# Kernel optimization log

Hardware: AMD Instinct MI355X
Metric: run time of the kernel (lower is better)

Reference implementation:

```python
import jax, jax.numpy as jnp
import numpy as np

H = 768
IMG_DIM = 2048
B = 256
S = 512
EPS = 1e-5


def _ln(x, g, b):
    mu = jnp.mean(x, axis=-1, keepdims=True)
    var = jnp.var(x, axis=-1, keepdims=True)
    return (x - mu) * jax.lax.rsqrt(var + EPS) * g + b


def setup_inputs() -> dict:
    key = jax.random.key(0)
    ks = jax.random.split(key, 16)
    std = 0.02
    d = {
        "text_features": jax.random.normal(ks[0], (B, S, H), jnp.float32),
        "image_features": jax.random.normal(ks[1], (B, IMG_DIM), jnp.float32),
        # projections (stored as [in, out]); attention/proj weights init N(0, 0.02), zero bias
        "Wp": jax.random.normal(ks[2], (IMG_DIM, H), jnp.float32) * std,
        "bp": jnp.zeros((H,), jnp.float32),
        "Wtq": jax.random.normal(ks[3], (H, H), jnp.float32) * std,
        "btq": jnp.zeros((H,), jnp.float32),
        "Wik": jax.random.normal(ks[4], (H, H), jnp.float32) * std,
        "bik": jnp.zeros((H,), jnp.float32),
        "Wiv": jax.random.normal(ks[5], (H, H), jnp.float32) * std,
        "biv": jnp.zeros((H,), jnp.float32),
        "Wiq": jax.random.normal(ks[6], (H, H), jnp.float32) * std,
        "biq": jnp.zeros((H,), jnp.float32),
        "Wtk": jax.random.normal(ks[7], (H, H), jnp.float32) * std,
        "btk": jnp.zeros((H,), jnp.float32),
        "Wtv": jax.random.normal(ks[8], (H, H), jnp.float32) * std,
        "btv": jnp.zeros((H,), jnp.float32),
        # layernorms
        "tn_g": jnp.ones((H,), jnp.float32),
        "tn_b": jnp.zeros((H,), jnp.float32),
        "in_g": jnp.ones((H,), jnp.float32),
        "in_b": jnp.zeros((H,), jnp.float32),
        # fusion MLP: Linear(2H,H) + LN + GELU
        "Wf": jax.random.normal(ks[9], (2 * H, H), jnp.float32) * (1.0 / np.sqrt(2 * H)),
        "bf": jnp.zeros((H,), jnp.float32),
        "fn_g": jnp.ones((H,), jnp.float32),
        "fn_b": jnp.zeros((H,), jnp.float32),
        # gate: Linear(2H,2) + softmax
        "Wg": jax.random.normal(ks[10], (2 * H, 2), jnp.float32) * (1.0 / np.sqrt(2 * H)),
        "bg": jnp.zeros((2,), jnp.float32),
    }
    return d


def reference(text_features, image_features, Wp, bp, Wtq, btq, Wik, bik, Wiv, biv,
              Wiq, biq, Wtk, btk, Wtv, btv, tn_g, tn_b, in_g, in_b,
              Wf, bf, fn_g, fn_b, Wg, bg):
    scale = 1.0 / jnp.sqrt(jnp.float32(H))
    cls_token = text_features[:, 0]                       # [B, H]
    img_projected = image_features @ Wp + bp              # [B, H]

    # image query attends over text tokens
    img_q = img_projected @ Wiq + biq                     # [B, H]
    text_k = jnp.einsum('bsd,de->bse', text_features, Wtk) + btk  # [B, S, H]
    text_v = jnp.einsum('bsd,de->bse', text_features, Wtv) + btv  # [B, S, H]
    scores = jnp.einsum('bd,bsd->bs', img_q, text_k) * scale      # [B, S]
    attn = jax.nn.softmax(scores, axis=-1)
    img_context = jnp.einsum('bs,bsd->bd', attn, text_v)          # [B, H]
    img_context = _ln(img_context + img_projected, in_g, in_b)

    # text CLS query attends over the single image token (softmax over 1 -> weight 1)
    text_q = cls_token @ Wtq + btq                        # [B, H]
    img_k = img_projected @ Wik + bik                     # [B, H]
    img_v = img_projected @ Wiv + biv                     # [B, H]
    t_scores = jnp.sum(text_q * img_k, axis=-1, keepdims=True) * scale  # [B, 1]
    t_attn = jax.nn.softmax(t_scores, axis=-1)            # == 1
    text_context = t_attn * img_v                         # [B, H]
    text_context = _ln(text_context + cls_token, tn_g, tn_b)

    combined = jnp.concatenate([text_context, img_context], axis=1)  # [B, 2H]
    gate = jax.nn.softmax(combined @ Wg + bg, axis=-1)               # [B, 2]
    weighted = jnp.concatenate([text_context * gate[:, 0:1],
                                img_context * gate[:, 1:2]], axis=1)  # [B, 2H]
    out = jax.nn.gelu(_ln(weighted @ Wf + bf, fn_g, fn_b), approximate=False)
    return out
```

## Files before the change

kernel.cpp:

```cpp
#include <hip/hip_runtime.h>
#include <hip/hip_bf16.h>

#define BD   256
#define SD   512
#define HD   768
#define IMGD 2048
#define TWOH 1536
constexpr float EPSV  = 1e-5f;
constexpr float SCALE = 0.036084391824351615f;
constexpr int   SPLIT = 4;
constexpr int   SBLK  = SD / SPLIT;

typedef __attribute__((ext_vector_type(8))) short short8;
typedef __attribute__((ext_vector_type(4))) float f32x4;

__device__ __forceinline__ short f2bs(float x) {
    __hip_bfloat16 h = __float2bfloat16(x);
    return __builtin_bit_cast(short, h);
}
__device__ __forceinline__ float4 f4sum(float4 a, float4 b) {
    return make_float4(a.x + b.x, a.y + b.y, a.z + b.z, a.w + b.w);
}
__device__ __forceinline__ float4 f4fma(float s, float4 v, float4 acc) {
    return make_float4(fmaf(s, v.x, acc.x), fmaf(s, v.y, acc.y),
                       fmaf(s, v.z, acc.z), fmaf(s, v.w, acc.w));
}

struct GemmSmem {
    __hip_bfloat16 As[2][64][40];
    __hip_bfloat16 Bs[2][64][40];
};

template<bool TRANSB, class AF, class BF>
__device__ __forceinline__ void gemm_core(GemmSmem& smem, AF aload, BF bload,
        const float* __restrict__ bias, float* __restrict__ C,
        int N, int m0, int n0, int NT) {
    const int tid  = threadIdx.x;
    const int w    = tid >> 6, lane = tid & 63;
    const int wr   = w >> 1,  wc   = w & 1;
    const int rsel = lane & 15, ks = (lane >> 4) * 8;
    const int arow = tid >> 2, akc = (tid & 3) * 8;
    const int bkk  = tid >> 3, bnc = (tid & 7) * 8;

    float4 a0v[2], a1v[2], b0v[2], b1v[2];

    auto issue = [&](int slot, int t) {
        aload(t, a0v[slot], a1v[slot]);
        bload(t, b0v[slot], b1v[slot]);
    };
    auto commit = [&](int buf, int slot) {
        short8 pk;
        pk[0]=f2bs(a0v[slot].x); pk[1]=f2bs(a0v[slot].y);
        pk[2]=f2bs(a0v[slot].z); pk[3]=f2bs(a0v[slot].w);
        pk[4]=f2bs(a1v[slot].x); pk[5]=f2bs(a1v[slot].y);
        pk[6]=f2bs(a1v[slot].z); pk[7]=f2bs(a1v[slot].w);
        *(short8*)&smem.As[buf][arow][akc] = pk;
        if (TRANSB) {
            short8 qk;
            qk[0]=f2bs(b0v[slot].x); qk[1]=f2bs(b0v[slot].y);
            qk[2]=f2bs(b0v[slot].z); qk[3]=f2bs(b0v[slot].w);
            qk[4]=f2bs(b1v[slot].x); qk[5]=f2bs(b1v[slot].y);
            qk[6]=f2bs(b1v[slot].z); qk[7]=f2bs(b1v[slot].w);
            *(short8*)&smem.Bs[buf][arow][akc] = qk;
        } else {
            smem.Bs[buf][bnc + 0][bkk] = __float2bfloat16(b0v[slot].x);
            smem.Bs[buf][bnc + 1][bkk] = __float2bfloat16(b0v[slot].y);
            smem.Bs[buf][bnc + 2][bkk] = __float2bfloat16(b0v[slot].z);
            smem.Bs[buf][bnc + 3][bkk] = __float2bfloat16(b0v[slot].w);
            smem.Bs[buf][bnc + 4][bkk] = __float2bfloat16(b1v[slot].x);
            smem.Bs[buf][bnc + 5][bkk] = __float2bfloat16(b1v[slot].y);
            smem.Bs[buf][bnc + 6][bkk] = __float2bfloat16(b1v[slot].z);
            smem.Bs[buf][bnc + 7][bkk] = __float2bfloat16(b1v[slot].w);
        }
    };

    f32x4 zero = {0.f, 0.f, 0.f, 0.f};
    f32x4 acc[2][2] = {{zero, zero}, {zero, zero}};

    issue(0, 0);
    commit(0, 0);
    if (NT > 1) issue(1, 1);
    __syncthreads();

    for (int t = 0; t < NT; ++t) {
        const int cur = t & 1;
        short8 A0 = *(const short8*)&smem.As[cur][wr * 32 + rsel][ks];
        short8 A1 = *(const short8*)&smem.As[cur][wr * 32 + 16 + rsel][ks];
        short8 B0 = *(const short8*)&smem.Bs[cur][wc * 32 + rsel][ks];
        short8 B1 = *(const short8*)&smem.Bs[cur][wc * 32 + 16 + rsel][ks];
        if (t + 1 < NT) commit(cur ^ 1, (t + 1) & 1);
        if (t + 2 < NT) issue(cur, t + 2);
        acc[0][0] = __builtin_amdgcn_mfma_f32_16x16x32_bf16(A0, B0, acc[0][0], 0, 0, 0);
        acc[0][1] = __builtin_amdgcn_mfma_f32_16x16x32_bf16(A0, B1, acc[0][1], 0, 0, 0);
        acc[1][0] = __builtin_amdgcn_mfma_f32_16x16x32_bf16(A1, B0, acc[1][0], 0, 0, 0);
        acc[1][1] = __builtin_amdgcn_mfma_f32_16x16x32_bf16(A1, B1, acc[1][1], 0, 0, 0);
        __syncthreads();
    }

    const int colb = lane & 15, rowb = (lane >> 4) * 4;
    #pragma unroll
    for (int fm = 0; fm < 2; ++fm)
        #pragma unroll
        for (int fn = 0; fn < 2; ++fn)
            #pragma unroll
            for (int r = 0; r < 4; ++r) {
                int row = m0 + wr * 32 + fm * 16 + rowb + r;
                int col = n0 + wc * 32 + fn * 16 + colb;
                float v = acc[fm][fn][r];
                if (bias) v += bias[col];
                C[(size_t)row * N + col] = v;
            }
}

__global__ __launch_bounds__(256) void stage1(const float* __restrict__ imgf,
                                              const float* __restrict__ Wp,
                                              const float* __restrict__ bp,
                                              const float* __restrict__ Wiq,
                                              const float* __restrict__ Wtk,
                                              const float* __restrict__ biq,
                                              float* __restrict__ Pp,
                                              float* __restrict__ Wqkp,
                                              float* __restrict__ v1) {
    __shared__ GemmSmem smem;
    const int blk = blockIdx.x, tid = threadIdx.x;
    const int arow = tid >> 2, akc = (tid & 3) * 8;
    const int bkk  = tid >> 3, bnc = (tid & 7) * 8;
    if (blk < 192) {
        const int part = blk / 48, tile = blk % 48;
        const int m0 = (tile / 12) * 64, n0 = (tile % 12) * 64, kbeg = part * 512;
        const float* ap = &imgf[(size_t)(m0 + arow) * IMGD + kbeg + akc];
        const float* bq = &Wp[(size_t)(kbeg + bkk) * HD + n0 + bnc];
        auto al = [&](int t, float4& v0, float4& v1_) {
            const float* p = ap + t * 32;
            v0 = *(const float4*)p; v1_ = *(const float4*)(p + 4);
        };
        auto bl = [&](int t, float4& v0, float4& v1_) {
            const float* p = bq + (size_t)t * 32 * HD;
            v0 = *(const float4*)p; v1_ = *(const float4*)(p + 4);
        };
        gemm_core<false>(smem, al, bl, part == 0 ? bp : nullptr,
                         Pp + (size_t)part * BD * HD, HD, m0, n0, 16);
    } else if (blk < 768) {
        const int b2 = blk - 192, part = b2 / 144, tile = b2 % 144;
        const int m0 = (tile / 12) * 64, n0 = (tile % 12) * 64, kbeg = part * 192;
        const float* ap = &Wiq[(size_t)(m0 + arow) * HD + kbeg + akc];
        const float* bq = &Wtk[(size_t)(n0 + arow) * HD + kbeg + akc];
        auto al = [&](int t, float4& v0, float4& v1_) {
            const float* p = ap + t * 32;
            v0 = *(const float4*)p; v1_ = *(const float4*)(p + 4);
        };
        auto bl = [&](int t, float4& v0, float4& v1_) {
            const float* p = bq + t * 32;
            v0 = *(const float4*)p; v1_ = *(const float4*)(p + 4);
        };
        gemm_core<true>(smem, al, bl, nullptr,
                        Wqkp + (size_t)part * HD * HD, HD, m0, n0, 6);
    } else {
        const int b2 = blk - 768;
        const int w = tid >> 6, lane = tid & 63;
        float bq[12];
        #pragma unroll
        for (int c = 0; c < 12; ++c) bq[c] = biq[c * 64 + lane];
        const int d0 = b2 * 64 + w * 16;
        for (int i = 0; i < 16; ++i) {
            const float* row = &Wtk[(size_t)(d0 + i) * HD];
            float p = 0.f;
            #pragma unroll
            for (int c = 0; c < 12; ++c) p = fmaf(row[c * 64 + lane], bq[c], p);
            #pragma unroll
            for (int off = 32; off > 0; off >>= 1) p += __shfl_xor(p, off);
            if (lane == 0) v1[d0 + i] = p;
        }
    }
}

__global__ __launch_bounds__(256) void stage2(const float* __restrict__ Pp,
                                              const float* __restrict__ Wqkp,
                                              const float* __restrict__ v1,
                                              const float* __restrict__ Wiv,
                                              const float* __restrict__ biv,
                                              float* __restrict__ qtp,
                                              float* __restrict__ ivp) {
    __shared__ GemmSmem smem;
    const int blk = blockIdx.x, tid = threadIdx.x;
    const int arow = tid >> 2, akc = (tid & 3) * 8;
    const int bkk  = tid >> 3, bnc = (tid & 7) * 8;
    const bool isqt = blk < 192;
    const int b2 = isqt ? blk : blk - 192;
    const int part = b2 / 48, tile = b2 % 48;
    const int m0 = (tile / 12) * 64, n0 = (tile % 12) * 64, kbeg = part * 192;

    const float* ap = &Pp[(size_t)(m0 + arow) * HD + kbeg + akc];
    auto al = [&](int t, float4& v0, float4& v1_) {
        const float* p = ap + t * 32;
        float4 x0 = *(const float4*)p, x1 = *(const float4*)(p + 4);
        #pragma unroll
        for (int q = 1; q < 4; ++q) {
            const float* r = p + (size_t)q * BD * HD;
            x0 = f4sum(x0, *(const float4*)r);
            x1 = f4sum(x1, *(const float4*)(r + 4));
        }
        v0 = x0; v1_ = x1;
    };
    if (isqt) {
        const float* bq = &Wqkp[(size_t)(kbeg + bkk) * HD + n0 + bnc];
        auto bl = [&](int t, float4& v0, float4& v1_) {
            const float* p = bq + (size_t)t * 32 * HD;
            float4 x0 = *(const float4*)p, x1 = *(const float4*)(p + 4);
            #pragma unroll
            for (int q = 1; q < 4; ++q) {
                const float* r = p + (size_t)q * HD * HD;
                x0 = f4sum(x0, *(const float4*)r);
                x1 = f4sum(x1, *(const float4*)(r + 4));
            }
            v0 = x0; v1_ = x1;
        };
        gemm_core<false>(smem, al, bl, part == 0 ? v1 : nullptr,
                         qtp + (size_t)part * BD * HD, HD, m0, n0, 6);
    } else {
        const float* bq = &Wiv[(size_t)(kbeg + bkk) * HD + n0 + bnc];
        auto bl = [&](int t, float4& v0, float4& v1_) {
            const float* p = bq + (size_t)t * 32 * HD;
            v0 = *(const float4*)p; v1_ = *(const float4*)(p + 4);
        };
        gemm_core<false>(smem, al, bl, part == 0 ? biv : nullptr,
                         ivp + (size_t)part * BD * HD, HD, m0, n0, 6);
    }
}

__global__ __launch_bounds__(256) void stream_attn(const float* __restrict__ tf,
                                                   const float* __restrict__ qtp,
                                                   float* __restrict__ pacc,
                                                   float* __restrict__ ml) {
    const int tid = threadIdx.x, w = tid >> 6, lane = tid & 63;
    const int item = blockIdx.x;
    const int b = item >> 2, sl = item & 3;
    __shared__ float sacc[4][HD];
    __shared__ float sm_[4], sl_[4];

    float q[12];
    {
        const float* qp = &qtp[b * HD];
        #pragma unroll
        for (int c = 0; c < 3; ++c) {
            float4 v = *(const float4*)&qp[c * 256 + 4 * lane];
            #pragma unroll
            for (int p = 1; p < 4; ++p)
                v = f4sum(v, *(const float4*)&qp[(size_t)p * BD * HD + c * 256 + 4 * lane]);
            q[c*4+0] = v.x; q[c*4+1] = v.y; q[c*4+2] = v.z; q[c*4+3] = v.w;
        }
    }
    float a[12];
    #pragma unroll
    for (int j = 0; j < 12; ++j) a[j] = 0.f;
    float m = -INFINITY, l = 0.f;

    const int r0 = sl * SBLK + w * (SBLK / 4);
    const float* base = &tf[((size_t)b * SD + r0) * HD];

    float tA[12], tB[12];
    auto loadrow = [&](int i, float* t) {
        const float* row = base + (size_t)i * HD;
        #pragma unroll
        for (int c = 0; c < 3; ++c) {
            float4 v = *(const float4*)&row[c * 256 + 4 * lane];
            t[c*4+0] = v.x; t[c*4+1] = v.y; t[c*4+2] = v.z; t[c*4+3] = v.w;
        }
    };
    auto process = [&](const float* t) {
        float p = 0.f;
        #pragma unroll
        for (int j = 0; j < 12; ++j) p = fmaf(t[j], q[j], p);
        #pragma unroll
        for (int off = 32; off > 0; off >>= 1) p += __shfl_xor(p, off);
        float score = p * SCALE;
        float mn = fmaxf(m, score);
        float eo = __expf(m - mn);
        float en = __expf(score - mn);
        l = fmaf(l, eo, en);
        #pragma unroll
        for (int j = 0; j < 12; ++j) a[j] = fmaf(a[j], eo, en * t[j]);
        m = mn;
    };

    loadrow(0, tA);
    for (int i = 0; i < 32; i += 2) {
        loadrow(i + 1, tB);
        process(tA);
        if (i + 2 < 32) loadrow(i + 2, tA);
        process(tB);
    }

    #pragma unroll
    for (int c = 0; c < 3; ++c)
        #pragma unroll
        for (int j = 0; j < 4; ++j)
            sacc[w][c * 256 + 4 * lane + j] = a[c * 4 + j];
    if (lane == 0) { sm_[w] = m; sl_[w] = l; }
    __syncthreads();
    float gm = fmaxf(fmaxf(sm_[0], sm_[1]), fmaxf(sm_[2], sm_[3]));
    float f0 = __expf(sm_[0] - gm), f1 = __expf(sm_[1] - gm);
    float f2 = __expf(sm_[2] - gm), f3 = __expf(sm_[3] - gm);
    float gl = f0 * sl_[0] + f1 * sl_[1] + f2 * sl_[2] + f3 * sl_[3];
    float* outp = &pacc[(size_t)item * HD];
    #pragma unroll
    for (int jj = 0; jj < 3; ++jj) {
        int c = jj * 256 + tid;
        outp[c] = f0 * sacc[0][c] + f1 * sacc[1][c] + f2 * sacc[2][c] + f3 * sacc[3][c];
    }
    if (tid == 0) { ml[item * 2] = gm; ml[item * 2 + 1] = gl; }
}

__global__ __launch_bounds__(256) void gemm_ctxv(const float* __restrict__ pacc,
                                                 const float* __restrict__ ml,
                                                 const float* __restrict__ Wtv,
                                                 const float* __restrict__ btv,
                                                 float* __restrict__ icpp) {
    __shared__ GemmSmem smem;
    __shared__ float wgt[64][SPLIT];
    const int tid = threadIdx.x;
    const int arow = tid >> 2, akc = (tid & 3) * 8;
    const int bkk  = tid >> 3, bnc = (tid & 7) * 8;
    const int part = blockIdx.x / 48, tile = blockIdx.x % 48;
    const int m0 = (tile / 12) * 64, n0 = (tile % 12) * 64, kbeg = part * 192;

    if (tid < 64) {
        const int gr = m0 + tid;
        float mv[SPLIT], lv[SPLIT];
        #pragma unroll
        for (int s = 0; s < SPLIT; ++s) {
            mv[s] = ml[(gr * SPLIT + s) * 2];
            lv[s] = ml[(gr * SPLIT + s) * 2 + 1];
        }
        float mx = fmaxf(fmaxf(mv[0], mv[1]), fmaxf(mv[2], mv[3]));
        float f[SPLIT], gl = 0.f;
        #pragma unroll
        for (int s = 0; s < SPLIT; ++s) { f[s] = __expf(mv[s] - mx); gl += f[s] * lv[s]; }
        float inv = 1.f / gl;
        #pragma unroll
        for (int s = 0; s < SPLIT; ++s) wgt[tid][s] = f[s] * inv;
    }
    __syncthreads();

    const float* ap = &pacc[(size_t)(m0 + arow) * SPLIT * HD + kbeg + akc];
    auto al = [&](int t, float4& v0, float4& v1_) {
        const float* p = ap + t * 32;
        float4 x0 = {0.f, 0.f, 0.f, 0.f}, x1 = {0.f, 0.f, 0.f, 0.f};
        #pragma unroll
        for (int s = 0; s < SPLIT; ++s) {
            float wv = wgt[arow][s];
            const float* r = p + (size_t)s * HD;
            x0 = f4fma(wv, *(const float4*)r, x0);
            x1 = f4fma(wv, *(const float4*)(r + 4), x1);
        }
        v0 = x0; v1_ = x1;
    };
    const float* bq = &Wtv[(size_t)(kbeg + bkk) * HD + n0 + bnc];
    auto bl = [&](int t, float4& v0, float4& v1_) {
        const float* p = bq + (size_t)t * 32 * HD;
        v0 = *(const float4*)p; v1_ = *(const float4*)(p + 4);
    };
    gemm_core<false>(smem, al, bl, part == 0 ? btv : nullptr,
                     icpp + (size_t)part * BD * HD, HD, m0, n0, 6);
}

__global__ __launch_bounds__(256) void gemm_wf(const float* __restrict__ wtd,
                                               const float* __restrict__ Wf,
                                               const float* __restrict__ bf,
                                               float* __restrict__ ybp) {
    __shared__ GemmSmem smem;
    const int tid = threadIdx.x;
    const int arow = tid >> 2, akc = (tid & 3) * 8;
    const int bkk  = tid >> 3, bnc = (tid & 7) * 8;
    const int part = blockIdx.x / 48, tile = blockIdx.x % 48;
    const int m0 = (tile / 12) * 64, n0 = (tile % 12) * 64, kbeg = part * 192;
    const float* ap = &wtd[(size_t)(m0 + arow) * TWOH + kbeg + akc];
    const float* bq = &Wf[(size_t)(kbeg + bkk) * HD + n0 + bnc];
    auto al = [&](int t, float4& v0, float4& v1_) {
        const float* p = ap + t * 32;
        v0 = *(const float4*)p; v1_ = *(const float4*)(p + 4);
    };
    auto bl = [&](int t, float4& v0, float4& v1_) {
        const float* p = bq + (size_t)t * 32 * HD;
        v0 = *(const float4*)p; v1_ = *(const float4*)(p + 4);
    };
    gemm_core<false>(smem, al, bl, part == 0 ? bf : nullptr,
                     ybp + (size_t)part * BD * HD, HD, m0, n0, 6);
}

__device__ __forceinline__ float block_sum256(float v, float* red, int w, int lane) {
    #pragma unroll
    for (int off = 32; off > 0; off >>= 1) v += __shfl_xor(v, off);
    __syncthreads();
    if (lane == 0) red[w] = v;
    __syncthreads();
    return red[0] + red[1] + red[2] + red[3];
}

__global__ __launch_bounds__(256) void fuse_small(const float* __restrict__ icpp,
                                                  const float* __restrict__ Pp,
                                                  const float* __restrict__ ivp,
                                                  const float* __restrict__ tf,
                                                  const float* __restrict__ in_g,
                                                  const float* __restrict__ in_b,
                                                  const float* __restrict__ tn_g,
                                                  const float* __restrict__ tn_b,
                                                  const float* __restrict__ Wg,
                                                  const float* __restrict__ bg,
                                                  float* __restrict__ wtd) {
    const int b = blockIdx.x, tid = threadIdx.x;
    const int w = tid >> 6, lane = tid & 63;
    __shared__ float red[4];
    float icv[3], tcv[3];
    #pragma unroll
    for (int j = 0; j < 3; ++j) {
        int c = j * 256 + tid;
        float pv = 0.f, ic = 0.f, iv = 0.f;
        #pragma unroll
        for (int q = 0; q < 4; ++q) {
            pv += Pp[(size_t)q * BD * HD + b * HD + c];
            ic += icpp[(size_t)q * BD * HD + b * HD + c];
            iv += ivp[(size_t)q * BD * HD + b * HD + c];
        }
        icv[j] = ic + pv;
        tcv[j] = iv + tf[(size_t)b * SD * HD + c];
    }
    float s_i  = block_sum256(icv[0] + icv[1] + icv[2], red, w, lane);
    float ss_i = block_sum256(icv[0]*icv[0] + icv[1]*icv[1] + icv[2]*icv[2], red, w, lane);
    float s_t  = block_sum256(tcv[0] + tcv[1] + tcv[2], red, w, lane);
    float ss_t = block_sum256(tcv[0]*tcv[0] + tcv[1]*tcv[1] + tcv[2]*tcv[2], red, w, lane);
    const float invh = 1.f / HD;
    float mu_i = s_i * invh, var_i = ss_i * invh - mu_i * mu_i;
    float mu_t = s_t * invh, var_t = ss_t * invh - mu_t * mu_t;
    float rs_i = rsqrtf(var_i + EPSV), rs_t = rsqrtf(var_t + EPSV);
    float icn[3], tcn[3];
    #pragma unroll
    for (int j = 0; j < 3; ++j) {
        int c = j * 256 + tid;
        icn[j] = (icv[j] - mu_i) * rs_i * in_g[c] + in_b[c];
        tcn[j] = (tcv[j] - mu_t) * rs_t * tn_g[c] + tn_b[c];
    }
    float z0p = 0.f, z1p = 0.f;
    #pragma unroll
    for (int j = 0; j < 3; ++j) {
        int c = j * 256 + tid;
        z0p += tcn[j] * Wg[c * 2 + 0] + icn[j] * Wg[(HD + c) * 2 + 0];
        z1p += tcn[j] * Wg[c * 2 + 1] + icn[j] * Wg[(HD + c) * 2 + 1];
    }
    float z0 = block_sum256(z0p, red, w, lane) + bg[0];
    float z1 = block_sum256(z1p, red, w, lane) + bg[1];
    float mx = fmaxf(z0, z1);
    float e0 = __expf(z0 - mx), e1 = __expf(z1 - mx);
    float inv = 1.f / (e0 + e1);
    float g0 = e0 * inv, g1 = e1 * inv;
    #pragma unroll
    for (int j = 0; j < 3; ++j) {
        int c = j * 256 + tid;
        wtd[(size_t)b * TWOH + c]      = tcn[j] * g0;
        wtd[(size_t)b * TWOH + HD + c] = icn[j] * g1;
    }
}

__global__ __launch_bounds__(256) void final_ln_gelu(const float* __restrict__ ybp,
                                                     const float* __restrict__ fn_g,
                                                     const float* __restrict__ fn_b,
                                                     float* __restrict__ out) {
    const int b = blockIdx.x, tid = threadIdx.x;
    const int w = tid >> 6, lane = tid & 63;
    __shared__ float red[4];
    float v[3];
    #pragma unroll
    for (int j = 0; j < 3; ++j) {
        int c = j * 256 + tid;
        float x = 0.f;
        #pragma unroll
        for (int q = 0; q < 8; ++q) x += ybp[(size_t)q * BD * HD + b * HD + c];
        v[j] = x;
    }
    float s  = block_sum256(v[0] + v[1] + v[2], red, w, lane);
    float ss = block_sum256(v[0]*v[0] + v[1]*v[1] + v[2]*v[2], red, w, lane);
    const float invh = 1.f / HD;
    float mu = s * invh, var = ss * invh - mu * mu;
    float rs = rsqrtf(var + EPSV);
    #pragma unroll
    for (int j = 0; j < 3; ++j) {
        int c = j * 256 + tid;
        float x = (v[j] - mu) * rs * fn_g[c] + fn_b[c];
        float g = 0.5f * x * (1.f + erff(x * 0.7071067811865476f));
        out[b * HD + c] = g;
    }
}

extern "C" void kernel_launch(void* const* d_in, const int* in_sizes, int n_in,
                              void* d_out, int out_size, void* d_ws, size_t ws_size,
                              hipStream_t stream) {
    const float* tf   = (const float*)d_in[0];
    const float* imgf = (const float*)d_in[1];
    const float* Wp   = (const float*)d_in[2];
    const float* bp   = (const float*)d_in[3];
    const float* Wiv  = (const float*)d_in[8];
    const float* biv  = (const float*)d_in[9];
    const float* Wiq  = (const float*)d_in[10];
    const float* biq  = (const float*)d_in[11];
    const float* Wtk  = (const float*)d_in[12];
    const float* Wtv  = (const float*)d_in[14];
    const float* btv  = (const float*)d_in[15];
    const float* tn_g = (const float*)d_in[16];
    const float* tn_b = (const float*)d_in[17];
    const float* in_g = (const float*)d_in[18];
    const float* in_b = (const float*)d_in[19];
    const float* Wf   = (const float*)d_in[20];
    const float* bff  = (const float*)d_in[21];
    const float* fn_g = (const float*)d_in[22];
    const float* fn_b = (const float*)d_in[23];
    const float* Wg   = (const float*)d_in[24];
    const float* bg   = (const float*)d_in[25];

    float* ws    = (float*)d_ws;
    float* Pp    = ws;
    float* Wqkp  = Pp    + 4 * BD * HD;
    float* v1    = Wqkp  + 4 * HD * HD;
    float* qtp   = v1    + HD;
    float* ivp   = qtp   + 4 * BD * HD;
    float* icpp  = ivp   + 4 * BD * HD;
    float* ybp   = icpp  + 4 * BD * HD;
    float* wtd   = ybp   + 8 * BD * HD;
    float* pacc  = wtd   + BD * TWOH;
    float* ml    = pacc  + (size_t)BD * SPLIT * HD;

    stage1<<<780, 256, 0, stream>>>(imgf, Wp, bp, Wiq, Wtk, biq, Pp, Wqkp, v1);
    stage2<<<384, 256, 0, stream>>>(Pp, Wqkp, v1, Wiv, biv, qtp, ivp);
    stream_attn<<<BD * SPLIT, 256, 0, stream>>>(tf, qtp, pacc, ml);
    gemm_ctxv<<<192, 256, 0, stream>>>(pacc, ml, Wtv, btv, icpp);
    fuse_small<<<BD, 256, 0, stream>>>(icpp, Pp, ivp, tf, in_g, in_b, tn_g, tn_b,
                                       Wg, bg, wtd);
    gemm_wf<<<384, 256, 0, stream>>>(wtd, Wf, bff, ybp);
    final_ln_gelu<<<BD, 256, 0, stream>>>(ybp, fn_g, fn_b, (float*)d_out);
}
```

Measured before the change: 146.7 us.

## Fuse seven kernel launches into one persistent megakernel with grid barriers

Replaces the seven separate kernel launches with a single persistent kernel of 512 blocks. The former stages become device-side phases separated by an atomic-counter grid barrier, and the counter is reset with a memset before each launch. This is meant to remove the launch and drain gaps between the small stages. In exchange it adds barrier spin cost, leaves blocks idle in phases with fewer work items, and depends on all 512 blocks being resident at once; a timeout in the barrier avoids a hang but could break correctness.

```diff
diff --git a/kernel.cpp b/kernel.cpp
--- a/kernel.cpp
+++ b/kernel.cpp
@@ -10,6 +10,7 @@
 constexpr float SCALE = 0.036084391824351615f;
 constexpr int   SPLIT = 4;
 constexpr int   SBLK  = SD / SPLIT;
+#define GRIDN 512u
 
 typedef __attribute__((ext_vector_type(8))) short short8;
 typedef __attribute__((ext_vector_type(4))) float f32x4;
@@ -30,6 +31,23 @@
     __hip_bfloat16 As[2][64][40];
     __hip_bfloat16 Bs[2][64][40];
 };
+
+__device__ __forceinline__ void gbar(unsigned* cnt, unsigned round) {
+    __syncthreads();
+    if (threadIdx.x == 0) {
+        __threadfence();
+        atomicAdd(cnt, 1u);
+        const unsigned target = round * GRIDN;
+        unsigned long long t0 = __builtin_amdgcn_s_memrealtime();
+        while (__hip_atomic_load(cnt, __ATOMIC_RELAXED,
+                                 __HIP_MEMORY_SCOPE_AGENT) < target) {
+            __builtin_amdgcn_s_sleep(8);
+            if (__builtin_amdgcn_s_memrealtime() - t0 > 10000000ull) break;
+        }
+        __threadfence();
+    }
+    __syncthreads();
+}
 
 template<bool TRANSB, class AF, class BF>
 __device__ __forceinline__ void gemm_core(GemmSmem& smem, AF aload, BF bload,
@@ -112,17 +130,12 @@
             }
 }
 
-__global__ __launch_bounds__(256) void stage1(const float* __restrict__ imgf,
-                                              const float* __restrict__ Wp,
-                                              const float* __restrict__ bp,
-                                              const float* __restrict__ Wiq,
-                                              const float* __restrict__ Wtk,
-                                              const float* __restrict__ biq,
-                                              float* __restrict__ Pp,
-                                              float* __restrict__ Wqkp,
-                                              float* __restrict__ v1) {
-    __shared__ GemmSmem smem;
-    const int blk = blockIdx.x, tid = threadIdx.x;
+__device__ void ph_stage1(GemmSmem& smem, int blk,
+        const float* __restrict__ imgf, const float* __restrict__ Wp,
+        const float* __restrict__ bp, const float* __restrict__ Wiq,
+        const float* __restrict__ Wtk, const float* __restrict__ biq,
+        float* __restrict__ Pp, float* __restrict__ Wqkp, float* __restrict__ v1) {
+    const int tid = threadIdx.x;
     const int arow = tid >> 2, akc = (tid & 3) * 8;
     const int bkk  = tid >> 3, bnc = (tid & 7) * 8;
     if (blk < 192) {
@@ -155,7 +168,7 @@
         };
         gemm_core<true>(smem, al, bl, nullptr,
                         Wqkp + (size_t)part * HD * HD, HD, m0, n0, 6);
-    } else {
+    } else if (blk < 780) {
         const int b2 = blk - 768;
         const int w = tid >> 6, lane = tid & 63;
         float bq[12];
@@ -174,15 +187,12 @@
     }
 }
 
-__global__ __launch_bounds__(256) void stage2(const float* __restrict__ Pp,
-                                              const float* __restrict__ Wqkp,
-                                              const float* __restrict__ v1,
-                                              const float* __restrict__ Wiv,
-                                              const float* __restrict__ biv,
-                                              float* __restrict__ qtp,
-                                              float* __restrict__ ivp) {
-    __shared__ GemmSmem smem;
-    const int blk = blockIdx.x, tid = threadIdx.x;
+__device__ void ph_stage2(GemmSmem& smem, int blk,
+        const float* __restrict__ Pp, const float* __restrict__ Wqkp,
+        const float* __restrict__ v1, const float* __restrict__ Wiv,
+        const float* __restrict__ biv, float* __restrict__ qtp,
+        float* __restrict__ ivp) {
+    const int tid = threadIdx.x;
     const int arow = tid >> 2, akc = (tid & 3) * 8;
     const int bkk  = tid >> 3, bnc = (tid & 7) * 8;
     const bool isqt = blk < 192;
@@ -228,15 +238,11 @@
     }
 }
 
-__global__ __launch_bounds__(256) void stream_attn(const float* __restrict__ tf,
-                                                   const float* __restrict__ qtp,
-                                                   float* __restrict__ pacc,
-                                                   float* __restrict__ ml) {
+__device__ void ph_attn(float (*sacc)[HD], float* sm_, float* sl_, int item,
+        const float* __restrict__ tf, const float* __restrict__ qtp,
+        float* __restrict__ pacc, float* __restrict__ ml) {
     const int tid = threadIdx.x, w = tid >> 6, lane = tid & 63;
-    const int item = blockIdx.x;
     const int b = item >> 2, sl = item & 3;
-    __shared__ float sacc[4][HD];
-    __shared__ float sm_[4], sl_[4];
 
     float q[12];
     {
@@ -309,19 +315,17 @@
         outp[c] = f0 * sacc[0][c] + f1 * sacc[1][c] + f2 * sacc[2][c] + f3 * sacc[3][c];
     }
     if (tid == 0) { ml[item * 2] = gm; ml[item * 2 + 1] = gl; }
-}
-
-__global__ __launch_bounds__(256) void gemm_ctxv(const float* __restrict__ pacc,
-                                                 const float* __restrict__ ml,
-                                                 const float* __restrict__ Wtv,
-                                                 const float* __restrict__ btv,
-                                                 float* __restrict__ icpp) {
-    __shared__ GemmSmem smem;
-    __shared__ float wgt[64][SPLIT];
+    __syncthreads();
+}
+
+__device__ void ph_ctxv(GemmSmem& smem, float (*wgt)[SPLIT], int blk,
+        const float* __restrict__ pacc, const float* __restrict__ ml,
+        const float* __restrict__ Wtv, const float* __restrict__ btv,
+        float* __restrict__ icpp) {
     const int tid = threadIdx.x;
     const int arow = tid >> 2, akc = (tid & 3) * 8;
     const int bkk  = tid >> 3, bnc = (tid & 7) * 8;
-    const int part = blockIdx.x / 48, tile = blockIdx.x % 48;
+    const int part = blk / 48, tile = blk % 48;
     const int m0 = (tile / 12) * 64, n0 = (tile % 12) * 64, kbeg = part * 192;
 
     if (tid < 64) {
@@ -364,15 +368,13 @@
                      icpp + (size_t)part * BD * HD, HD, m0, n0, 6);
 }
 
-__global__ __launch_bounds__(256) void gemm_wf(const float* __restrict__ wtd,
-                                               const float* __restrict__ Wf,
-                                               const float* __restrict__ bf,
-                                               float* __restrict__ ybp) {
-    __shared__ GemmSmem smem;
+__device__ void ph_wf(GemmSmem& smem, int blk,
+        const float* __restrict__ wtd, const float* __restrict__ Wf,
+        const float* __restrict__ Wfb, float* __restrict__ ybp) {
     const int tid = threadIdx.x;
     const int arow = tid >> 2, akc = (tid & 3) * 8;
     const int bkk  = tid >> 3, bnc = (tid & 7) * 8;
-    const int part = blockIdx.x / 48, tile = blockIdx.x % 48;
+    const int part = blk / 48, tile = blk % 48;
     const int m0 = (tile / 12) * 64, n0 = (tile % 12) * 64, kbeg = part * 192;
     const float* ap = &wtd[(size_t)(m0 + arow) * TWOH + kbeg + akc];
     const float* bq = &Wf[(size_t)(kbeg + bkk) * HD + n0 + bnc];
@@ -384,7 +386,7 @@
         const float* p = bq + (size_t)t * 32 * HD;
         v0 = *(const float4*)p; v1_ = *(const float4*)(p + 4);
     };
-    gemm_core<false>(smem, al, bl, part == 0 ? bf : nullptr,
+    gemm_core<false>(smem, al, bl, part == 0 ? Wfb : nullptr,
                      ybp + (size_t)part * BD * HD, HD, m0, n0, 6);
 }
 
@@ -397,20 +399,15 @@
     return red[0] + red[1] + red[2] + red[3];
 }
 
-__global__ __launch_bounds__(256) void fuse_small(const float* __restrict__ icpp,
-                                                  const float* __restrict__ Pp,
-                                                  const float* __restrict__ ivp,
-                                                  const float* __restrict__ tf,
-                                                  const float* __restrict__ in_g,
-                                                  const float* __restrict__ in_b,
-                                                  const float* __restrict__ tn_g,
-                                                  const float* __restrict__ tn_b,
-                                                  const float* __restrict__ Wg,
-                                                  const float* __restrict__ bg,
-                                                  float* __restrict__ wtd) {
-    const int b = blockIdx.x, tid = threadIdx.x;
+__device__ void ph_fuse(float* red, int b,
+        const float* __restrict__ icpp, const float* __restrict__ Pp,
+        const float* __restrict__ ivp, const float* __restrict__ tf,
+        const float* __restrict__ in_g, const float* __restrict__ in_b,
+        const float* __restrict__ tn_g, const float* __restrict__ tn_b,
+        const float* __restrict__ Wg, const float* __restrict__ bg,
+        float* __restrict__ wtd) {
+    const int tid = threadIdx.x;
     const int w = tid >> 6, lane = tid & 63;
-    __shared__ float red[4];
     float icv[3], tcv[3];
     #pragma unroll
     for (int j = 0; j < 3; ++j) {
@@ -461,13 +458,11 @@
     }
 }
 
-__global__ __launch_bounds__(256) void final_ln_gelu(const float* __restrict__ ybp,
-                                                     const float* __restrict__ fn_g,
-                                                     const float* __restrict__ fn_b,
-                                                     float* __restrict__ out) {
-    const int b = blockIdx.x, tid = threadIdx.x;
+__device__ void ph_final(float* red, int b,
+        const float* __restrict__ ybp, const float* __restrict__ fn_g,
+        const float* __restrict__ fn_b, float* __restrict__ out) {
+    const int tid = threadIdx.x;
     const int w = tid >> 6, lane = tid & 63;
-    __shared__ float red[4];
     float v[3];
     #pragma unroll
     for (int j = 0; j < 3; ++j) {
@@ -489,6 +484,44 @@
         float g = 0.5f * x * (1.f + erff(x * 0.7071067811865476f));
         out[b * HD + c] = g;
     }
+}
+
+struct MegaParams {
+    const float *tf, *imgf, *Wp, *bp, *Wiv, *biv, *Wiq, *biq, *Wtk, *Wtv, *btv,
+                *tn_g, *tn_b, *in_g, *in_b, *Wf, *Wfb, *fn_g, *fn_b, *Wg, *bg;
+    float *Pp, *Wqkp, *v1, *qtp, *ivp, *icpp, *ybp, *wtd, *pacc, *ml, *out;
+    unsigned* cnt;
+};
+
+__global__ __launch_bounds__(256, 2) void mega(MegaParams P) {
+    __shared__ __align__(16) char arena[sizeof(GemmSmem)];
+    __shared__ float wgt[64][SPLIT];
+    __shared__ float redm[4];
+    GemmSmem& smem = *reinterpret_cast<GemmSmem*>(arena);
+    float (*sacc)[HD] = reinterpret_cast<float(*)[HD]>(arena);
+    float* sm_ = reinterpret_cast<float*>(arena + 12288);
+    float* sl_ = reinterpret_cast<float*>(arena + 12304);
+    const int blk = blockIdx.x;
+    unsigned* cnt = P.cnt;
+
+    for (int vb = blk; vb < 780; vb += (int)GRIDN)
+        ph_stage1(smem, vb, P.imgf, P.Wp, P.bp, P.Wiq, P.Wtk, P.biq,
+                  P.Pp, P.Wqkp, P.v1);
+    gbar(cnt, 1);
+    if (blk < 384) ph_stage2(smem, blk, P.Pp, P.Wqkp, P.v1, P.Wiv, P.biv,
+                             P.qtp, P.ivp);
+    gbar(cnt, 2);
+    for (int it = blk; it < BD * SPLIT; it += (int)GRIDN)
+        ph_attn(sacc, sm_, sl_, it, P.tf, P.qtp, P.pacc, P.ml);
+    gbar(cnt, 3);
+    if (blk < 192) ph_ctxv(smem, wgt, blk, P.pacc, P.ml, P.Wtv, P.btv, P.icpp);
+    gbar(cnt, 4);
+    if (blk < 256) ph_fuse(redm, blk, P.icpp, P.Pp, P.ivp, P.tf, P.in_g, P.in_b,
+                           P.tn_g, P.tn_b, P.Wg, P.bg, P.wtd);
+    gbar(cnt, 5);
+    if (blk < 384) ph_wf(smem, blk, P.wtd, P.Wf, P.Wfb, P.ybp);
+    gbar(cnt, 6);
+    if (blk < 256) ph_final(redm, blk, P.ybp, P.fn_g, P.fn_b, P.out);
 }
 
 extern "C" void kernel_launch(void* const* d_in, const int* in_sizes, int n_in,
@@ -527,13 +560,20 @@
     float* wtd   = ybp   + 8 * BD * HD;
     float* pacc  = wtd   + BD * TWOH;
     float* ml    = pacc  + (size_t)BD * SPLIT * HD;
-
-    stage1<<<780, 256, 0, stream>>>(imgf, Wp, bp, Wiq, Wtk, biq, Pp, Wqkp, v1);
-    stage2<<<384, 256, 0, stream>>>(Pp, Wqkp, v1, Wiv, biv, qtp, ivp);
-    stream_attn<<<BD * SPLIT, 256, 0, stream>>>(tf, qtp, pacc, ml);
-    gemm_ctxv<<<192, 256, 0, stream>>>(pacc, ml, Wtv, btv, icpp);
-    fuse_small<<<BD, 256, 0, stream>>>(icpp, Pp, ivp, tf, in_g, in_b, tn_g, tn_b,
-                                       Wg, bg, wtd);
-    gemm_wf<<<384, 256, 0, stream>>>(wtd, Wf, bff, ybp);
-    final_ln_gelu<<<BD, 256, 0, stream>>>(ybp, fn_g, fn_b, (float*)d_out);
-}
+    unsigned* cnt = (unsigned*)(ml + (size_t)BD * SPLIT * 2);
+
+    MegaParams prm;
+    prm.tf = tf; prm.imgf = imgf; prm.Wp = Wp; prm.bp = bp;
+    prm.Wiv = Wiv; prm.biv = biv; prm.Wiq = Wiq; prm.biq = biq;
+    prm.Wtk = Wtk; prm.Wtv = Wtv; prm.btv = btv;
+    prm.tn_g = tn_g; prm.tn_b = tn_b; prm.in_g = in_g; prm.in_b = in_b;
+    prm.Wf = Wf; prm.Wfb = bff; prm.fn_g = fn_g; prm.fn_b = fn_b;
+    prm.Wg = Wg; prm.bg = bg;
+    prm.Pp = Pp; prm.Wqkp = Wqkp; prm.v1 = v1; prm.qtp = qtp; prm.ivp = ivp;
+    prm.icpp = icpp; prm.ybp = ybp; prm.wtd = wtd; prm.pacc = pacc; prm.ml = ml;
+    prm.out = (float*)d_out;
+    prm.cnt = cnt;
+
+    hipMemsetAsync(cnt, 0, sizeof(unsigned), stream);
+    mega<<<dim3((int)GRIDN), dim3(256), 0, stream>>>(prm);
+}
```

Measured after the change: 469.3 us. +219.9%, slower.
